# Optimization experiments

Measured on AMD Instinct MI355X. Metric: run time of the kernel, lower is better.

## Reference

```python
import jax, jax.numpy as jnp
import numpy as np

L = 16          # n_levels
FPL = 2         # n_features_per_level
T = 2 ** 22     # hash table size
N_MIN = 16.0    # base_resolution
BB = 1.26       # per_level_scale
PI2 = jnp.uint32(2654435761)
N_PTS = 262144

# cubic Hermite basis matrix B (as in the torch module)
B_MAT = jnp.array([[1, 0, 0, 0],
                   [0, 0, 1, 0],
                   [-3, 3, -2, -1],
                   [2, -2, 1, 1]], dtype=jnp.float32)


def setup_inputs() -> dict:
    key = jax.random.key(0)
    k1, k2 = jax.random.split(key)
    x = jax.random.uniform(k1, (N_PTS, 2), dtype=jnp.float32)
    hash_table = jax.random.uniform(k2, (T, FPL, L), dtype=jnp.float32) * 2e-4 - 1e-4
    return {"x": x, "hash_table": hash_table}


def reference(x, hash_table):
    # per-level resolutions [L]
    NL = jnp.floor(N_MIN * BB ** jnp.arange(L, dtype=jnp.float32))
    xNL = x[:, :, None] * NL                      # [N, 2, L]
    xNL_floor = xNL.astype(jnp.int32)             # trunc == floor for x in [0,1)
    local = xNL - xNL_floor.astype(jnp.float32)   # [N, 2, L] fractional coords

    # 4x4 stencil: original local_node offsets (-1..2) + 1 -> 0..3
    offs = jnp.arange(4, dtype=jnp.int32)
    gx = xNL_floor[:, 0, :][:, None, None, :] + offs[None, :, None, None]  # [N,4,1,L]
    gy = xNL_floor[:, 1, :][:, None, None, :] + offs[None, None, :, None]  # [N,1,4,L]

    # spatial hash; low 22 bits of the int64 product equal those of the uint32 product,
    # and xor/mod only read low bits, so uint32 arithmetic matches the torch int64 math
    h = (gx.astype(jnp.uint32) * jnp.uint32(1)) ^ (gy.astype(jnp.uint32) * PI2)
    hij = (h % jnp.uint32(T)).astype(jnp.int32)   # [N, 4, 4, L]

    # gather per-level features: [N, 4, 4, L, FPL]
    f = hash_table[hij, :, jnp.arange(L)]

    # finite-difference derivatives on the stencil
    fy = (f[:, :, 2:] - f[:, :, :2]) * 0.5                 # [N,4,2,L,FPL]
    fx = (f[:, 2:] - f[:, :2]) * 0.5                       # [N,2,4,L,FPL]
    fxy = (fy[:, 2:] - fy[:, :2] + fx[:, :, 2:] - fx[:, :, :2]) * 0.25  # [N,2,2,L,FPL]
    fi = f[:, 1:3, 1:3]                                    # [N,2,2,L,FPL]
    Fm = jnp.concatenate([jnp.concatenate([fi, fy[:, 1:3]], axis=2),
                          jnp.concatenate([fx[:, :, 1:3], fxy], axis=2)], axis=1)  # [N,4,4,L,FPL]

    # Hermite weights: wx = xpow @ B, wy = ypow @ B (per point, per level)
    p = jnp.arange(4, dtype=jnp.float32)
    xpow = local[:, 0, :][:, None, :] ** p[None, :, None]  # [N,4,L]
    ypow = local[:, 1, :][:, None, :] ** p[None, :, None]  # [N,4,L]
    wx = jnp.einsum('nbl,bc->ncl', xpow, B_MAT)
    wy = jnp.einsum('ndl,dg->ngl', ypow, B_MAT)

    # out[n,l,f] = wx^T F wy, then flatten levels x features
    out = jnp.einsum('ncl,ncglf,ngl->nlf', wx, Fm, wy)     # [N, L, FPL]
    return out.reshape(out.shape[0], L * FPL)
```

## Files before the change

### kernel.cpp

```cpp
#include <hip/hip_runtime.h>
#include <stdint.h>

#define T_MASK 4194303u
#define PI2_C  2654435761u
#define NBKT   16384

__constant__ float c_NL[16] = {
    16.f, 20.f, 25.f, 32.f, 40.f, 50.f, 64.f, 80.f,
    101.f, 128.f, 161.f, 203.f, 256.f, 322.f, 406.f, 512.f
};

__device__ __forceinline__ uint32_t part1by1(uint32_t v) {
    v &= 0xffu;
    v = (v | (v << 4)) & 0x0F0Fu;
    v = (v | (v << 2)) & 0x3333u;
    v = (v | (v << 1)) & 0x5555u;
    return v;
}

__global__ __launch_bounds__(256) void zero_counts(uint32_t* counts) {
    int i = blockIdx.x * 256 + threadIdx.x;
    if (i < NBKT) counts[i] = 0;
}

__global__ __launch_bounds__(256) void hist_kernel(
    const float* __restrict__ x, uint32_t* __restrict__ keys,
    uint32_t* __restrict__ counts, int npts)
{
    int i = blockIdx.x * 256 + threadIdx.x;
    if (i >= npts) return;
    float px = x[2 * i], py = x[2 * i + 1];
    int cx = (int)(px * 128.f); cx = cx < 0 ? 0 : (cx > 127 ? 127 : cx);
    int cy = (int)(py * 128.f); cy = cy < 0 ? 0 : (cy > 127 ? 127 : cy);
    uint32_t key = part1by1((uint32_t)cx) | (part1by1((uint32_t)cy) << 1);
    keys[i] = key;
    atomicAdd(&counts[key], 1u);
}

__global__ __launch_bounds__(1024) void scan_kernel(uint32_t* __restrict__ counts) {
    __shared__ uint32_t sums[1024];
    int t = threadIdx.x;
    uint32_t local[NBKT / 1024];
    uint32_t s = 0;
    #pragma unroll
    for (int i = 0; i < NBKT / 1024; ++i) {
        local[i] = counts[t * (NBKT / 1024) + i];
        s += local[i];
    }
    sums[t] = s;
    __syncthreads();
    for (int off = 1; off < 1024; off <<= 1) {
        uint32_t v = (t >= off) ? sums[t - off] : 0u;
        __syncthreads();
        sums[t] += v;
        __syncthreads();
    }
    uint32_t run = (t > 0) ? sums[t - 1] : 0u;
    #pragma unroll
    for (int i = 0; i < NBKT / 1024; ++i) {
        uint32_t c = local[i];
        counts[t * (NBKT / 1024) + i] = run;
        run += c;
    }
}

__global__ __launch_bounds__(256) void scatter_kernel(
    const uint32_t* __restrict__ keys, uint32_t* __restrict__ offsets,
    uint32_t* __restrict__ order, int npts)
{
    int i = blockIdx.x * 256 + threadIdx.x;
    if (i >= npts) return;
    uint32_t pos = atomicAdd(&offsets[keys[i]], 1u);
    order[pos] = (uint32_t)i;
}

__global__ __launch_bounds__(256) void enc_cubic_kernel(
    const float* __restrict__ x,
    const float* __restrict__ ht,
    const uint32_t* __restrict__ order,
    float* __restrict__ out,
    int npts)
{
    uint32_t bid = blockIdx.x;
    uint32_t nb = gridDim.x;
    if ((nb & 7u) == 0u) {
        uint32_t chunk = nb >> 3;
        bid = (bid & 7u) * chunk + (bid >> 3);
    }
    uint32_t tid = bid * 256u + threadIdx.x;
    uint32_t w = tid >> 6;
    uint32_t lane = tid & 63u;
    uint32_t g = w >> 4;
    uint32_t l = (w + g) & 15u;
    uint32_t r = g * 64u + lane;
    if (r >= (uint32_t)npts) return;
    int n = (int)order[r];

    float NL = c_NL[l];
    float px = x[2 * n];
    float py = x[2 * n + 1];

    float xs = px * NL;
    float ys = py * NL;
    int ix = (int)xs;
    int iy = (int)ys;
    float tx = xs - (float)ix;
    float ty = ys - (float)iy;

    float tx2 = tx * tx, tx3 = tx2 * tx;
    float ty2 = ty * ty, ty3 = ty2 * ty;
    float wxa[4], wya[4];
    wxa[0] = -0.5f * tx + tx2 - 0.5f * tx3;
    wxa[1] = 1.0f - 2.5f * tx2 + 1.5f * tx3;
    wxa[2] = 0.5f * tx + 2.0f * tx2 - 1.5f * tx3;
    wxa[3] = -0.5f * tx2 + 0.5f * tx3;
    wya[0] = -0.5f * ty + ty2 - 0.5f * ty3;
    wya[1] = 1.0f - 2.5f * ty2 + 1.5f * ty3;
    wya[2] = 0.5f * ty + 2.0f * ty2 - 1.5f * ty3;
    wya[3] = -0.5f * ty2 + 0.5f * ty3;

    uint32_t hx[4], hy[4];
    #pragma unroll
    for (int i = 0; i < 4; ++i) hx[i] = (uint32_t)(ix + i);
    #pragma unroll
    for (int j = 0; j < 4; ++j) hy[j] = (uint32_t)(iy + j) * PI2_C;

    const float* base = ht + l;
    float acc0 = 0.f, acc1 = 0.f;
    #pragma unroll
    for (int j = 0; j < 4; ++j) {
        float r0 = 0.f, r1 = 0.f;
        #pragma unroll
        for (int i = 0; i < 4; ++i) {
            uint32_t h = (hx[i] ^ hy[j]) & T_MASK;
            const float* p = base + (size_t)h * 32u;
            r0 += wxa[i] * p[0];
            r1 += wxa[i] * p[16];
        }
        acc0 += wya[j] * r0;
        acc1 += wya[j] * r1;
    }

    float2* o = (float2*)(out + (size_t)n * 32 + l * 2);
    *o = make_float2(acc0, acc1);
}

extern "C" void kernel_launch(void* const* d_in, const int* in_sizes, int n_in,
                              void* d_out, int out_size, void* d_ws, size_t ws_size,
                              hipStream_t stream) {
    const float* x  = (const float*)d_in[0];
    const float* ht = (const float*)d_in[1];
    float* out = (float*)d_out;
    int npts = in_sizes[0] / 2;

    uint32_t* counts = (uint32_t*)d_ws;
    uint32_t* keys   = counts + NBKT;
    uint32_t* order  = keys + npts;

    int pb = (npts + 255) / 256;
    zero_counts<<<(NBKT + 255) / 256, 256, 0, stream>>>(counts);
    hist_kernel<<<pb, 256, 0, stream>>>(x, keys, counts, npts);
    scan_kernel<<<1, 1024, 0, stream>>>(counts);
    scatter_kernel<<<pb, 256, 0, stream>>>(keys, counts, order, npts);

    int total = npts * 16;
    int blocks = (total + 255) / 256;
    enc_cubic_kernel<<<blocks, 256, 0, stream>>>(x, ht, order, out, npts);
}
```

Measured before the change: 739.7 us.

## Process all levels per thread in a loop instead of thread per level

Maps one thread to one point and iterates over the 16 levels with a rotated starting level, instead of launching one thread per point-level pair. This removes redundant loads of the order index and coordinates and computes the output row address once per point. It cuts the thread count sixteenfold, which reduces occupancy and the number of outstanding random gathers that hide memory latency.

```diff
diff --git a/kernel.cpp b/kernel.cpp
--- a/kernel.cpp
+++ b/kernel.cpp
@@ -74,7 +74,7 @@
     order[pos] = (uint32_t)i;
 }
 
-__global__ __launch_bounds__(256) void enc_cubic_kernel(
+__global__ __launch_bounds__(256) void enc_cubic_pp_kernel(
     const float* __restrict__ x,
     const float* __restrict__ ht,
     const uint32_t* __restrict__ order,
@@ -87,62 +87,56 @@
         uint32_t chunk = nb >> 3;
         bid = (bid & 7u) * chunk + (bid >> 3);
     }
-    uint32_t tid = bid * 256u + threadIdx.x;
-    uint32_t w = tid >> 6;
-    uint32_t lane = tid & 63u;
-    uint32_t g = w >> 4;
-    uint32_t l = (w + g) & 15u;
-    uint32_t r = g * 64u + lane;
+    uint32_t r = bid * 256u + threadIdx.x;
     if (r >= (uint32_t)npts) return;
     int n = (int)order[r];
+    float2 pxy = *(const float2*)(x + 2u * (size_t)n);
+    float px = pxy.x;
+    float py = pxy.y;
+    float* orow = out + (size_t)n * 32u;
+    uint32_t lrot = (r >> 6) & 15u;
 
-    float NL = c_NL[l];
-    float px = x[2 * n];
-    float py = x[2 * n + 1];
+    #pragma unroll 1
+    for (int k = 0; k < 16; ++k) {
+        uint32_t l = ((uint32_t)k + lrot) & 15u;
+        float NL = c_NL[l];
+        float xs = px * NL;
+        float ys = py * NL;
+        int ix = (int)xs;
+        int iy = (int)ys;
+        float tx = xs - (float)ix;
+        float ty = ys - (float)iy;
 
-    float xs = px * NL;
-    float ys = py * NL;
-    int ix = (int)xs;
-    int iy = (int)ys;
-    float tx = xs - (float)ix;
-    float ty = ys - (float)iy;
+        float tx2 = tx * tx, tx3 = tx2 * tx;
+        float ty2 = ty * ty, ty3 = ty2 * ty;
+        float wxa[4], wya[4];
+        wxa[0] = -0.5f * tx + tx2 - 0.5f * tx3;
+        wxa[1] = 1.0f - 2.5f * tx2 + 1.5f * tx3;
+        wxa[2] = 0.5f * tx + 2.0f * tx2 - 1.5f * tx3;
+        wxa[3] = -0.5f * tx2 + 0.5f * tx3;
+        wya[0] = -0.5f * ty + ty2 - 0.5f * ty3;
+        wya[1] = 1.0f - 2.5f * ty2 + 1.5f * ty3;
+        wya[2] = 0.5f * ty + 2.0f * ty2 - 1.5f * ty3;
+        wya[3] = -0.5f * ty2 + 0.5f * ty3;
 
-    float tx2 = tx * tx, tx3 = tx2 * tx;
-    float ty2 = ty * ty, ty3 = ty2 * ty;
-    float wxa[4], wya[4];
-    wxa[0] = -0.5f * tx + tx2 - 0.5f * tx3;
-    wxa[1] = 1.0f - 2.5f * tx2 + 1.5f * tx3;
-    wxa[2] = 0.5f * tx + 2.0f * tx2 - 1.5f * tx3;
-    wxa[3] = -0.5f * tx2 + 0.5f * tx3;
-    wya[0] = -0.5f * ty + ty2 - 0.5f * ty3;
-    wya[1] = 1.0f - 2.5f * ty2 + 1.5f * ty3;
-    wya[2] = 0.5f * ty + 2.0f * ty2 - 1.5f * ty3;
-    wya[3] = -0.5f * ty2 + 0.5f * ty3;
-
-    uint32_t hx[4], hy[4];
-    #pragma unroll
-    for (int i = 0; i < 4; ++i) hx[i] = (uint32_t)(ix + i);
-    #pragma unroll
-    for (int j = 0; j < 4; ++j) hy[j] = (uint32_t)(iy + j) * PI2_C;
-
-    const float* base = ht + l;
-    float acc0 = 0.f, acc1 = 0.f;
-    #pragma unroll
-    for (int j = 0; j < 4; ++j) {
-        float r0 = 0.f, r1 = 0.f;
+        const float* base = ht + l;
+        float acc0 = 0.f, acc1 = 0.f;
         #pragma unroll
-        for (int i = 0; i < 4; ++i) {
-            uint32_t h = (hx[i] ^ hy[j]) & T_MASK;
-            const float* p = base + (size_t)h * 32u;
-            r0 += wxa[i] * p[0];
-            r1 += wxa[i] * p[16];
+        for (int j = 0; j < 4; ++j) {
+            uint32_t hy = (uint32_t)(iy + j) * PI2_C;
+            float r0 = 0.f, r1 = 0.f;
+            #pragma unroll
+            for (int i = 0; i < 4; ++i) {
+                uint32_t h = (((uint32_t)(ix + i)) ^ hy) & T_MASK;
+                const float* p = base + (size_t)h * 32u;
+                r0 += wxa[i] * p[0];
+                r1 += wxa[i] * p[16];
+            }
+            acc0 += wya[j] * r0;
+            acc1 += wya[j] * r1;
         }
-        acc0 += wya[j] * r0;
-        acc1 += wya[j] * r1;
+        *(float2*)(orow + 2u * l) = make_float2(acc0, acc1);
     }
-
-    float2* o = (float2*)(out + (size_t)n * 32 + l * 2);
-    *o = make_float2(acc0, acc1);
 }
 
 extern "C" void kernel_launch(void* const* d_in, const int* in_sizes, int n_in,
@@ -163,7 +157,5 @@
     scan_kernel<<<1, 1024, 0, stream>>>(counts);
     scatter_kernel<<<pb, 256, 0, stream>>>(keys, counts, order, npts);
 
-    int total = npts * 16;
-    int blocks = (total + 255) / 256;
-    enc_cubic_kernel<<<blocks, 256, 0, stream>>>(x, ht, order, out, npts);
+    enc_cubic_pp_kernel<<<pb, 256, 0, stream>>>(x, ht, order, out, npts);
 }
```

Measured after the change: 775.4 us. 4.8% more time.
